# Performance work log

Hardware: AMD Instinct MI355X
Metric: run time of the kernel (lower is better)

The kernel has to match this reference:

```python
import jax, jax.numpy as jnp
import numpy as np

B, S, G, E, H = 256, 100000, 18000, 600000, 256


def setup_inputs() -> dict:
    key = jax.random.key(0)
    ks = jax.random.split(key, 8)
    x = jax.random.normal(ks[0], (B, S), dtype=jnp.float32)
    # bipartite SNP->gene edge list (connectivity from the tsv)
    snp_idx = jax.random.randint(ks[1], (E,), 0, S)
    gene_idx = jax.random.randint(ks[2], (E,), 0, G)
    # SparseLinear: one learned weight per edge, plus per-gene bias
    edge_w = jax.random.normal(ks[3], (E,), dtype=jnp.float32) * (1.0 / np.sqrt(E / G))
    gene_bias = jax.random.normal(ks[4], (G,), dtype=jnp.float32) * 0.01
    # interaction_layer: Linear(G -> H)
    W1 = jax.random.normal(ks[5], (H, G), dtype=jnp.float32) / np.sqrt(G)
    b1 = jnp.zeros((H,), dtype=jnp.float32)
    # phenotype_layer: Linear(H -> 1)
    W2 = jax.random.normal(ks[6], (1, H), dtype=jnp.float32) / np.sqrt(H)
    b2 = jnp.zeros((1,), dtype=jnp.float32)
    return {"x": x, "snp_idx": snp_idx, "gene_idx": gene_idx, "edge_w": edge_w,
            "gene_bias": gene_bias, "W1": W1, "b1": b1, "W2": W2, "b2": b2}


def reference(x, snp_idx, gene_idx, edge_w, gene_bias, W1, b1, W2, b2):
    # SparseLinear: gather SNP values per edge, weight, scatter-add into genes
    vals = x[:, snp_idx] * edge_w                                  # [B, E]
    gene = jnp.zeros((x.shape[0], gene_bias.shape[0]), x.dtype)
    gene = gene.at[:, gene_idx].add(vals) + gene_bias              # [B, G]
    h = gene @ W1.T + b1                                           # [B, H]
    out = h @ W2.T + b2                                            # [B, 1]
    return out.reshape(-1)                                         # [B]
```

## Files before the change

kernel.cpp:

```cpp
#include <hip/hip_runtime.h>


__global__ void compute_v_kernel(const float* __restrict__ W1,
                                 const float* __restrict__ W2,
                                 const float* __restrict__ b1,
                                 const float* __restrict__ b2,
                                 const float* __restrict__ gene_bias,
                                 float* __restrict__ v,
                                 float* __restrict__ Cptr,
                                 int G, int H)
{
    __shared__ float red[256];
    const int tid = threadIdx.x;
    const int gl  = tid & 63;
    const int hg  = tid >> 6;
    const int g   = blockIdx.x * 64 + gl;

    float acc = 0.f;
    if (g < G) {
        for (int h = hg; h < H; h += 4) {
            acc += W2[h] * W1[(size_t)h * G + g];
        }
    }
    red[tid] = acc;
    __syncthreads();

    float cc = 0.f;
    if (hg == 0 && g < G) {
        float vg = red[gl] + red[64 + gl] + red[128 + gl] + red[192 + gl];
        v[g] = vg;
        cc = gene_bias[g] * vg;
    }
    if (blockIdx.x == 0) {
        for (int h = tid; h < H; h += blockDim.x) cc += W2[h] * b1[h];
        if (tid == 0) cc += b2[0];
    }
    __syncthreads();
    red[tid] = cc;
    __syncthreads();
    for (int s = 128; s > 0; s >>= 1) {
        if (tid < s) red[tid] += red[tid + s];
        __syncthreads();
    }
    if (tid == 0) atomicAdd(Cptr, red[0]);
}

__global__ void scatter_u_kernel(const int* __restrict__ snp_idx,
                                 const int* __restrict__ gene_idx,
                                 const float* __restrict__ edge_w,
                                 const float* __restrict__ v,
                                 float* __restrict__ u,
                                 int E)
{
    int i = blockIdx.x * blockDim.x + threadIdx.x;
    if (i < E) {
        atomicAdd(&u[snp_idx[i]], edge_w[i] * v[gene_idx[i]]);
    }
}

__global__ __launch_bounds__(1024)
void output_kernel(const float* __restrict__ x,
                   const float* __restrict__ u,
                   const float* __restrict__ Cptr,
                   float* __restrict__ out,
                   int S)
{
    const int b   = blockIdx.x;
    const int tid = threadIdx.x;
    const float* xr = x + (size_t)b * S;
    float acc = 0.f;

    if ((S & 3) == 0) {
        const float4* x4 = (const float4*)xr;
        const float4* u4 = (const float4*)u;
        const int S4 = S >> 2;
        for (int i = tid; i < S4; i += (int)blockDim.x) {
            float4 a = x4[i];
            float4 c = u4[i];
            acc += a.x * c.x + a.y * c.y + a.z * c.z + a.w * c.w;
        }
    } else {
        for (int i = tid; i < S; i += (int)blockDim.x) acc += xr[i] * u[i];
    }

    for (int off = 32; off > 0; off >>= 1) acc += __shfl_down(acc, off, 64);
    __shared__ float wsum[16];
    const int wave = tid >> 6;
    const int lane = tid & 63;
    if (lane == 0) wsum[wave] = acc;
    __syncthreads();
    if (tid == 0) {
        float t = 0.f;
        const int nwaves = (int)blockDim.x >> 6;
        for (int w = 0; w < nwaves; ++w) t += wsum[w];
        out[b] = t + Cptr[0];
    }
}

extern "C" void kernel_launch(void* const* d_in, const int* in_sizes, int n_in,
                              void* d_out, int out_size, void* d_ws, size_t ws_size,
                              hipStream_t stream)
{
    const float* x         = (const float*)d_in[0];
    const int*   snp_idx   = (const int*)  d_in[1];
    const int*   gene_idx  = (const int*)  d_in[2];
    const float* edge_w    = (const float*)d_in[3];
    const float* gene_bias = (const float*)d_in[4];
    const float* W1        = (const float*)d_in[5];
    const float* b1        = (const float*)d_in[6];
    const float* W2        = (const float*)d_in[7];
    const float* b2        = (const float*)d_in[8];
    float* out = (float*)d_out;

    const int B = out_size;
    const int E = in_sizes[1];
    const int G = in_sizes[4];
    const int H = in_sizes[6];
    const int S = in_sizes[0] / B;

    float* u    = (float*)d_ws;
    float* v    = u + S;
    float* Cptr = v + G;

    hipMemsetAsync(d_ws, 0, (size_t)(S + G + 1) * sizeof(float), stream);

    const int nbv = (G + 63) / 64;
    compute_v_kernel<<<nbv, 256, 0, stream>>>(W1, W2, b1, b2, gene_bias, v, Cptr, G, H);

    const int nbs = (E + 255) / 256;
    scatter_u_kernel<<<nbs, 256, 0, stream>>>(snp_idx, gene_idx, edge_w, v, u, E);

    output_kernel<<<B, 1024, 0, stream>>>(x, u, Cptr, out, S);
}
```

Measured before the change: 243.2 us.

## Fold workspace zeroing into v kernel, drop scalar atomic, vectorize edge scatter

Removes the separate hipMemsetAsync by having compute_v_kernel zero the u buffer with float4 stores in a grid-stride loop. The global atomicAdd for the constant term is replaced by per-block partial sums, which every output block re-reduces as part of its row dot product. The scatter kernel now loads four edges per thread with int4 and float4 loads. This saves one launch and the serialized atomics, at the cost of each output block redundantly reading the partials and of fewer threads issuing the scatter atomics.

```diff
diff --git a/kernel.cpp b/kernel.cpp
--- a/kernel.cpp
+++ b/kernel.cpp
@@ -7,14 +7,23 @@
                                  const float* __restrict__ b2,
                                  const float* __restrict__ gene_bias,
                                  float* __restrict__ v,
-                                 float* __restrict__ Cptr,
-                                 int G, int H)
+                                 float* __restrict__ Cpart,
+                                 float4* __restrict__ u4,
+                                 int G, int H, int nU4)
 {
     __shared__ float red[256];
     const int tid = threadIdx.x;
-    const int gl  = tid & 63;
-    const int hg  = tid >> 6;
-    const int g   = blockIdx.x * 64 + gl;
+
+    {
+        const int gid = blockIdx.x * 256 + tid;
+        const int tot = gridDim.x * 256;
+        const float4 z = make_float4(0.f, 0.f, 0.f, 0.f);
+        for (int i = gid; i < nU4; i += tot) u4[i] = z;
+    }
+
+    const int gl = tid & 63;
+    const int hg = tid >> 6;
+    const int g  = blockIdx.x * 64 + gl;
 
     float acc = 0.f;
     if (g < G) {
@@ -32,7 +41,7 @@
         cc = gene_bias[g] * vg;
     }
     if (blockIdx.x == 0) {
-        for (int h = tid; h < H; h += blockDim.x) cc += W2[h] * b1[h];
+        for (int h = tid; h < H; h += 256) cc += W2[h] * b1[h];
         if (tid == 0) cc += b2[0];
     }
     __syncthreads();
@@ -42,7 +51,7 @@
         if (tid < s) red[tid] += red[tid + s];
         __syncthreads();
     }
-    if (tid == 0) atomicAdd(Cptr, red[0]);
+    if (tid == 0) Cpart[blockIdx.x] = red[0];
 }
 
 __global__ void scatter_u_kernel(const int* __restrict__ snp_idx,
@@ -52,36 +61,44 @@
                                  float* __restrict__ u,
                                  int E)
 {
-    int i = blockIdx.x * blockDim.x + threadIdx.x;
-    if (i < E) {
-        atomicAdd(&u[snp_idx[i]], edge_w[i] * v[gene_idx[i]]);
+    const int i4 = blockIdx.x * blockDim.x + threadIdx.x;
+    const int base = i4 * 4;
+    if (base + 3 < E) {
+        const int4   s = *(const int4*)  (snp_idx  + base);
+        const int4   g = *(const int4*)  (gene_idx + base);
+        const float4 w = *(const float4*)(edge_w   + base);
+        atomicAdd(&u[s.x], w.x * v[g.x]);
+        atomicAdd(&u[s.y], w.y * v[g.y]);
+        atomicAdd(&u[s.z], w.z * v[g.z]);
+        atomicAdd(&u[s.w], w.w * v[g.w]);
+    } else {
+        for (int i = base; i < E; ++i)
+            atomicAdd(&u[snp_idx[i]], edge_w[i] * v[gene_idx[i]]);
     }
 }
 
 __global__ __launch_bounds__(1024)
 void output_kernel(const float* __restrict__ x,
                    const float* __restrict__ u,
-                   const float* __restrict__ Cptr,
+                   const float* __restrict__ Cpart,
+                   int nC,
                    float* __restrict__ out,
                    int S)
 {
     const int b   = blockIdx.x;
     const int tid = threadIdx.x;
+    float acc = (tid < nC) ? Cpart[tid] : 0.f;
+
     const float* xr = x + (size_t)b * S;
-    float acc = 0.f;
-
-    if ((S & 3) == 0) {
-        const float4* x4 = (const float4*)xr;
-        const float4* u4 = (const float4*)u;
-        const int S4 = S >> 2;
-        for (int i = tid; i < S4; i += (int)blockDim.x) {
-            float4 a = x4[i];
-            float4 c = u4[i];
-            acc += a.x * c.x + a.y * c.y + a.z * c.z + a.w * c.w;
-        }
-    } else {
-        for (int i = tid; i < S; i += (int)blockDim.x) acc += xr[i] * u[i];
+    const int S4 = S >> 2;
+    const float4* x4 = (const float4*)xr;
+    const float4* u4 = (const float4*)u;
+    for (int i = tid; i < S4; i += 1024) {
+        float4 a = x4[i];
+        float4 c = u4[i];
+        acc += a.x * c.x + a.y * c.y + a.z * c.z + a.w * c.w;
     }
+    for (int i = (S4 << 2) + tid; i < S; i += 1024) acc += xr[i] * u[i];
 
     for (int off = 32; off > 0; off >>= 1) acc += __shfl_down(acc, off, 64);
     __shared__ float wsum[16];
@@ -91,9 +108,8 @@
     __syncthreads();
     if (tid == 0) {
         float t = 0.f;
-        const int nwaves = (int)blockDim.x >> 6;
-        for (int w = 0; w < nwaves; ++w) t += wsum[w];
-        out[b] = t + Cptr[0];
+        for (int w = 0; w < 16; ++w) t += wsum[w];
+        out[b] = t;
     }
 }
 
@@ -118,17 +134,18 @@
     const int H = in_sizes[6];
     const int S = in_sizes[0] / B;
 
-    float* u    = (float*)d_ws;
-    float* v    = u + S;
-    float* Cptr = v + G;
+    const int nU4 = (S + 3) / 4;
+    float* u     = (float*)d_ws;
+    float* v     = u + (size_t)nU4 * 4;
+    const int nbv = (G + 63) / 64;
+    float* Cpart = v + G;
 
-    hipMemsetAsync(d_ws, 0, (size_t)(S + G + 1) * sizeof(float), stream);
+    compute_v_kernel<<<nbv, 256, 0, stream>>>(W1, W2, b1, b2, gene_bias,
+                                              v, Cpart, (float4*)u, G, H, nU4);
 
-    const int nbv = (G + 63) / 64;
-    compute_v_kernel<<<nbv, 256, 0, stream>>>(W1, W2, b1, b2, gene_bias, v, Cptr, G, H);
+    const int nE4 = (E + 3) / 4;
+    scatter_u_kernel<<<(nE4 + 255) / 256, 256, 0, stream>>>(snp_idx, gene_idx, edge_w,
+                                                            v, u, E);
 
-    const int nbs = (E + 255) / 256;
-    scatter_u_kernel<<<nbs, 256, 0, stream>>>(snp_idx, gene_idx, edge_w, v, u, E);
-
-    output_kernel<<<B, 1024, 0, stream>>>(x, u, Cptr, out, S);
+    output_kernel<<<B, 1024, 0, stream>>>(x, u, Cpart, nbv, out, S);
 }
```

After: 241.2 us. About the same (-0.8%).
